# Kernel optimization log

Measured on AMD Instinct MI355X. Metric: run time of the kernel, lower is better.

Reference implementation:

```python
import jax, jax.numpy as jnp
import numpy as np

KH = KW = 3
STRIDE = 1
PAD = 1
DIL = 1


def setup_inputs() -> dict:
    key = jax.random.key(0)
    k0, k1, k2, k3 = jax.random.split(key, 4)
    B, C, H, W = 4, 64, 128, 128
    Cout = 64
    K = KH * KW
    x = jax.random.normal(k0, (B, C, H, W), jnp.float32)
    # main deform-conv weight [Cout, C, KH, KW]
    weight = jax.random.normal(k1, (Cout, C, KH, KW), jnp.float32) * (1.0 / np.sqrt(C * K))
    bias = jax.random.normal(k2, (Cout,), jnp.float32) * 0.01
    # offset-generating conv: 2*K output channels (dy,dx per kernel tap), deform_groups=1
    offset_weight = jax.random.normal(k3, (2 * K, C, KH, KW), jnp.float32) * 0.01
    offset_bias = jnp.zeros((2 * K,), jnp.float32)
    return {"x": x, "weight": weight, "bias": bias,
            "offset_weight": offset_weight, "offset_bias": offset_bias}


def _conv(x, w, b):
    out = jax.lax.conv_general_dilated(
        x, w, (STRIDE, STRIDE), [(PAD, PAD), (PAD, PAD)],
        rhs_dilation=(DIL, DIL), dimension_numbers=("NCHW", "OIHW", "NCHW"))
    return out + b[None, :, None, None]


def _deform_conv(x, weight, bias, offset_weight, offset_bias):
    B, C, H, W = x.shape
    K = KH * KW
    # offsets from sibling conv: [B, 2K, Ho, Wo], layout (k, [dy, dx]) interleaved
    offs = _conv(x, offset_weight, offset_bias)
    Ho, Wo = offs.shape[2], offs.shape[3]
    offs = offs.reshape(B, K, 2, Ho, Wo)
    dy, dx = offs[:, :, 0], offs[:, :, 1]          # [B, K, Ho, Wo]

    # base sampling grid: output pixel origin + dilated kernel tap + learned offset
    base_h = (jnp.arange(Ho) * STRIDE - PAD).astype(x.dtype)
    base_w = (jnp.arange(Wo) * STRIDE - PAD).astype(x.dtype)
    ky, kx = jnp.meshgrid(jnp.arange(KH) * DIL, jnp.arange(KW) * DIL, indexing="ij")
    ky = ky.reshape(K).astype(x.dtype)
    kx = kx.reshape(K).astype(x.dtype)
    py = base_h[None, None, :, None] + ky[None, :, None, None] + dy   # [B,K,Ho,Wo]
    px = base_w[None, None, None, :] + kx[None, :, None, None] + dx

    y0 = jnp.floor(py)
    x0 = jnp.floor(px)
    ly = py - y0   # fractional weights
    lx = px - x0
    y0i = y0.astype(jnp.int32)
    x0i = x0.astype(jnp.int32)

    x_flat = x.reshape(B, C, H * W)

    def gather(yi, xi):
        # zero padding outside the image
        valid = (yi >= 0) & (yi < H) & (xi >= 0) & (xi < W)
        yc = jnp.clip(yi, 0, H - 1)
        xc = jnp.clip(xi, 0, W - 1)
        idx = (yc * W + xc).reshape(B, -1)          # [B, K*Ho*Wo]
        g = jax.vmap(lambda f, i: f[:, i])(x_flat, idx)  # [B, C, K*Ho*Wo]
        g = g.reshape(B, C, K, Ho, Wo)
        return g * valid[:, None].astype(x.dtype)

    v00 = gather(y0i,     x0i)
    v01 = gather(y0i,     x0i + 1)
    v10 = gather(y0i + 1, x0i)
    v11 = gather(y0i + 1, x0i + 1)

    wy = ly[:, None]   # [B,1,K,Ho,Wo]
    wx = lx[:, None]
    patches = (v00 * (1 - wy) * (1 - wx) + v01 * (1 - wy) * wx
               + v10 * wy * (1 - wx) + v11 * wy * wx)   # [B,C,K,Ho,Wo]

    Cout = weight.shape[0]
    out = jnp.einsum("bckhw,ock->bohw", patches, weight.reshape(Cout, C, K))
    return out + bias[None, :, None, None]


def reference(x, weight, bias, offset_weight, offset_bias):
    return _deform_conv(x, weight, bias, offset_weight, offset_bias)
```

## Files before the change

### kernel.cpp

```cpp
#include <hip/hip_runtime.h>

#define B_   4
#define C_   64
#define H_   128
#define W_   128
#define OC_  64
#define K_   9
#define OCH_ 18
#define CK_  576

#define S_    104
#define WCOLS 768
#define XSW   72
#define XSH   7
#define XSC   (XSH*XSW)
#define XSC1  (3*XSW)
#define XSB   4096
#define NS2   1008
#define NS1   432

#define WPAD_HALFS  (OC_*WCOLS)
#define W0PAD_HALFS (32*WCOLS)
#define ZPAGE_BYTE  (2*WPAD_HALFS + 2*W0PAD_HALFS)

using half8v  = __attribute__((ext_vector_type(8))) _Float16;
using half2v  = __attribute__((ext_vector_type(2))) _Float16;
using float4v = __attribute__((ext_vector_type(4))) float;

#define GLDS16(SRC, DST)                                              \
    __builtin_amdgcn_global_load_lds(                                 \
        (__attribute__((address_space(1))) void*)(SRC),               \
        (__attribute__((address_space(3))) void*)(DST), 16, 0, 0)

__global__ void k0_prep(const float* __restrict__ w, const float* __restrict__ ow,
                        _Float16* __restrict__ wpad, _Float16* __restrict__ w0pad,
                        float* __restrict__ zp) {
    if (blockIdx.x == 0 && threadIdx.x < 64) zp[threadIdx.x] = 0.f;
    int i = blockIdx.x * 256 + threadIdx.x;
    if (i < OC_ * WCOLS) {
        int oc = i / WCOLS, col = i - oc * WCOLS;
        int cc = col / 96, r = col - cc * 96;
        int kk = r >> 3, cl = r & 7;
        float v = 0.f;
        if (kk < 9) v = w[oc * CK_ + (cc * 8 + cl) * 9 + kk];
        wpad[i] = (_Float16)v;
    } else {
        int j = i - OC_ * WCOLS;
        if (j < 32 * WCOLS) {
            int rr = j / WCOLS, col = j - rr * WCOLS;
            int cc = col / 96, r = col - cc * 96;
            int kk = r >> 3, cl = r & 7;
            float v = 0.f;
            if (rr < OCH_ && kk < 9) v = ow[rr * CK_ + (cc * 8 + cl) * 9 + kk];
            w0pad[j] = (_Float16)v;
        }
    }
}

__global__ __launch_bounds__(256, 3) void k_fused(
    const float* __restrict__ x, const _Float16* __restrict__ wpad,
    const _Float16* __restrict__ w0pad, const float* __restrict__ bias,
    const float* __restrict__ ob, const float* __restrict__ zp,
    float* __restrict__ out)
{
    __shared__ __align__(16) float    xs[2 * XSB];
    __shared__ __align__(16) _Float16 Pl[64 * S_];
    __shared__ float offs_lds[OCH_ * 64];

    const int g   = blockIdx.x;
    const int xcd = g & 7;
    const int n   = g >> 3;
    const int hb  = n & 1;
    const int hol = (n >> 1) & 15;
    const int b   = n >> 5;
    const int ho  = xcd * 16 + hol;

    const int t = threadIdx.x, lane = t & 63, w = t >> 6;
    const int lr = lane & 15, q = lane >> 4;
    const int lpix = w * 16 + lr;
    const int po   = hb * 64 + lpix;
    const int start = hb * 64 - 4;
    const float* xb = x + ((long)b << 20);

    for (int i = t; i < 64 * 12; i += 256) {
        int row = i / 12, j = i - row * 12;
        *(unsigned*)&Pl[row * S_ + 72 + 2 * j] = 0u;
    }

    int g1o[2]; bool g1k[2], g1v[2];
#pragma unroll
    for (int s = 0; s < 2; s++) {
        int idx = t + 256 * s;
        g1v[s] = idx < NS1;
        int ii = g1v[s] ? idx : 0;
        int c  = ii / 54, rj = ii - c * 54;
        int r3 = rj / 18, jc = rj - r3 * 18;
        int gy = ho - 1 + r3, gx = start + 4 * jc;
        g1k[s] = ((unsigned)gy < (unsigned)H_) && (gx >= 0) && (gx + 3 < W_);
        g1o[s] = (c << 14) + (gy << 7) + gx;
    }
    int g2o[4]; bool g2k[4], g2v[4];
#pragma unroll
    for (int s = 0; s < 4; s++) {
        int idx = t + 256 * s;
        g2v[s] = idx < NS2;
        int ii = g2v[s] ? idx : 0;
        int c  = ii / 126, rj = ii - c * 126;
        int r  = rj / 18, jc = rj - r * 18;
        int gy = ho - 3 + r, gx = start + 4 * jc;
        g2k[s] = ((unsigned)gy < (unsigned)H_) && (gx >= 0) && (gx + 3 < W_);
        g2o[s] = (c << 14) + (gy << 7) + gx;
    }

#pragma unroll
    for (int s = 0; s < 2; s++) if (g1v[s])
        GLDS16(g1k[s] ? (xb + g1o[s]) : zp, xs + 4 * (t + 256 * s));

    float4v oa0 = {0.f,0.f,0.f,0.f}, oa1 = {0.f,0.f,0.f,0.f};

    for (int cc = 0; cc < 8; cc++) {
        __syncthreads();
        if (cc < 7) {
            float* dst = xs + ((cc + 1) & 1) * XSB;
            const float* srcb = xb + ((long)(cc + 1) << 17);
#pragma unroll
            for (int s = 0; s < 2; s++) if (g1v[s])
                GLDS16(g1k[s] ? (srcb + g1o[s]) : zp, dst + 4 * (t + 256 * s));
        }
        {
            const float* b0 = xs + (cc & 1) * XSB + (2 * q) * XSC1;
            const float* b1 = b0 + XSC1;
#pragma unroll
            for (int ky = 0; ky < 3; ky++) {
#pragma unroll
                for (int kx = 0; kx < 3; kx++) {
                    float u0 = b0[ky * XSW + lpix + 3 + kx];
                    float u1 = b1[ky * XSW + lpix + 3 + kx];
                    half2v hv = {(_Float16)u0, (_Float16)u1};
                    *(half2v*)&Pl[lpix * S_ + (ky * 3 + kx) * 8 + 2 * q] = hv;
                }
            }
        }
        __syncthreads();
#pragma unroll
        for (int ks = 0; ks < 3; ks++) {
            half8v a0 = *(const half8v*)&w0pad[lr * WCOLS + cc * 96 + ks * 32 + q * 8];
            half8v a1 = *(const half8v*)&w0pad[(16 + lr) * WCOLS + cc * 96 + ks * 32 + q * 8];
            half8v bv = *(const half8v*)&Pl[lpix * S_ + ks * 32 + q * 8];
            oa0 = __builtin_amdgcn_mfma_f32_16x16x32_f16(a0, bv, oa0, 0, 0, 0);
            oa1 = __builtin_amdgcn_mfma_f32_16x16x32_f16(a1, bv, oa1, 0, 0, 0);
        }
    }

#pragma unroll
    for (int r = 0; r < 4; r++) {
        int ch = q * 4 + r;
        offs_lds[ch * 64 + lpix] = oa0[r] + ob[ch];
    }
#pragma unroll
    for (int r = 0; r < 4; r++) {
        int ch = 16 + q * 4 + r;
        if (ch < OCH_) offs_lds[ch * 64 + lpix] = oa1[r] + ob[ch];
    }
    __syncthreads();

#pragma unroll
    for (int s = 0; s < 4; s++) if (g2v[s])
        GLDS16(g2k[s] ? (xb + g2o[s]) : zp, xs + 4 * (t + 256 * s));

    unsigned moff[9];
    float mw0[9], mw1[9], mw2[9], mw3[9];
    unsigned okm = 0;
#pragma unroll
    for (int kk = 0; kk < 9; kk++) {
        int ky = kk / 3, kx = kk - 3 * ky;
        float dy = offs_lds[(2 * kk) * 64 + lpix];
        float dx = offs_lds[(2 * kk + 1) * 64 + lpix];
        float py = (float)(ho - 1 + ky) + dy;
        float px = (float)(po - 1 + kx) + dx;
        float fy = floorf(py), fx = floorf(px);
        float ly = py - fy, lx = px - fx;
        int y0 = (int)fy, x0 = (int)fx;
        int y1 = y0 + 1, x1 = x0 + 1;
        float vy0 = ((unsigned)y0 < (unsigned)H_) ? 1.f : 0.f;
        float vy1 = ((unsigned)y1 < (unsigned)H_) ? 1.f : 0.f;
        float vx0 = ((unsigned)x0 < (unsigned)W_) ? 1.f : 0.f;
        float vx1 = ((unsigned)x1 < (unsigned)W_) ? 1.f : 0.f;
        float w00 = (1.f - ly) * (1.f - lx) * vy0 * vx0;
        float w01 = (1.f - ly) * lx * vy0 * vx1;
        float w10 = ly * (1.f - lx) * vy1 * vx0;
        float w11 = ly * lx * vy1 * vx1;
        int cy0 = min(max(y0, 0), H_ - 1);
        int cy1 = min(max(y1, 0), H_ - 1);
        int xl  = min(max(x0, 0), W_ - 2);
        bool noswap = (x0 == xl);
        mw0[kk] = noswap ? w00 : w01;
        mw1[kk] = noswap ? w01 : w00;
        mw2[kk] = noswap ? w10 : w11;
        mw3[kk] = noswap ? w11 : w10;
        int sy0 = cy0 - (ho - 3);
        int sy1 = cy1 - (ho - 3);
        int sx  = xl - start;
        bool ok = ((unsigned)sy0 < (unsigned)XSH) && ((unsigned)sy1 < (unsigned)XSH)
               && ((unsigned)sx < (unsigned)(XSW - 1));
        okm |= (ok ? 1u : 0u) << kk;
        moff[kk] = (unsigned)(sy0 * XSW + sx) | ((unsigned)(sy1 * XSW + sx) << 16);
    }

    float4v a00 = {0.f,0.f,0.f,0.f}, a01 = {0.f,0.f,0.f,0.f};
    float4v a10 = {0.f,0.f,0.f,0.f}, a11 = {0.f,0.f,0.f,0.f};
    const int wm = w & 1, wn = w >> 1;

    for (int cc = 0; cc < 8; cc++) {
        __syncthreads();
        if (cc < 7) {
            float* dst = xs + ((cc + 1) & 1) * XSB;
            const float* srcb = xb + ((long)(cc + 1) << 17);
#pragma unroll
            for (int s = 0; s < 4; s++) if (g2v[s])
                GLDS16(g2k[s] ? (srcb + g2o[s]) : zp, dst + 4 * (t + 256 * s));
        }
        const float* xs0 = xs + (cc & 1) * XSB + (2 * q) * XSC;
        const float* xs1 = xs0 + XSC;
        if (__all(okm == 0x1FFu)) {
#pragma unroll
            for (int kk = 0; kk < 9; kk++) {
                int A  = (int)(moff[kk] & 0xFFFFu);
                int Bo = (int)(moff[kk] >> 16);
                float p0 = xs0[A] * mw0[kk] + xs0[A + 1] * mw1[kk]
                         + xs0[Bo] * mw2[kk] + xs0[Bo + 1] * mw3[kk];
                float p1 = xs1[A] * mw0[kk] + xs1[A + 1] * mw1[kk]
                         + xs1[Bo] * mw2[kk] + xs1[Bo + 1] * mw3[kk];
                half2v hv = {(_Float16)p0, (_Float16)p1};
                *(half2v*)&Pl[lpix * S_ + kk * 8 + 2 * q] = hv;
            }
        } else {
            const float* xc0 = xb + ((long)(cc * 8 + 2 * q) << 14);
            const float* xc1 = xc0 + (1 << 14);
#pragma unroll
            for (int kk = 0; kk < 9; kk++) {
                int ky = kk / 3, kx = kk - 3 * ky;
                float dy = offs_lds[(2 * kk) * 64 + lpix];
                float dx = offs_lds[(2 * kk + 1) * 64 + lpix];
                float py = (float)(ho - 1 + ky) + dy;
                float px = (float)(po - 1 + kx) + dx;
                int y0 = (int)floorf(py), x0 = (int)floorf(px);
                int cy0 = min(max(y0, 0), H_ - 1);
                int cy1 = min(max(y0 + 1, 0), H_ - 1);
                int xl  = min(max(x0, 0), W_ - 2);
                int ga = (cy0 << 7) + xl, gb = (cy1 << 7) + xl;
                float p0 = xc0[ga] * mw0[kk] + xc0[ga + 1] * mw1[kk]
                         + xc0[gb] * mw2[kk] + xc0[gb + 1] * mw3[kk];
                float p1 = xc1[ga] * mw0[kk] + xc1[ga + 1] * mw1[kk]
                         + xc1[gb] * mw2[kk] + xc1[gb + 1] * mw3[kk];
                half2v hv = {(_Float16)p0, (_Float16)p1};
                *(half2v*)&Pl[lpix * S_ + kk * 8 + 2 * q] = hv;
            }
        }
        __syncthreads();
#pragma unroll
        for (int ks = 0; ks < 3; ks++) {
            half8v A0 = *(const half8v*)&wpad[(wm * 32 + lr) * WCOLS + cc * 96 + ks * 32 + q * 8];
            half8v A1 = *(const half8v*)&wpad[(wm * 32 + 16 + lr) * WCOLS + cc * 96 + ks * 32 + q * 8];
            half8v B0 = *(const half8v*)&Pl[(wn * 32 + lr) * S_ + ks * 32 + q * 8];
            half8v B1 = *(const half8v*)&Pl[(wn * 32 + 16 + lr) * S_ + ks * 32 + q * 8];
            a00 = __builtin_amdgcn_mfma_f32_16x16x32_f16(A0, B0, a00, 0, 0, 0);
            a01 = __builtin_amdgcn_mfma_f32_16x16x32_f16(A0, B1, a01, 0, 0, 0);
            a10 = __builtin_amdgcn_mfma_f32_16x16x32_f16(A1, B0, a10, 0, 0, 0);
            a11 = __builtin_amdgcn_mfma_f32_16x16x32_f16(A1, B1, a11, 0, 0, 0);
        }
    }

    const int pixc = hb * 64 + wn * 32 + lr;
#pragma unroll
    for (int r = 0; r < 4; r++) {
        int oc0 = wm * 32 + q * 4 + r;
        int oc1 = oc0 + 16;
        float* o0 = out + (((long)(b * OC_ + oc0)) << 14) + (ho << 7);
        float* o1 = out + (((long)(b * OC_ + oc1)) << 14) + (ho << 7);
        o0[pixc]      = a00[r] + bias[oc0];
        o0[pixc + 16] = a01[r] + bias[oc0];
        o1[pixc]      = a10[r] + bias[oc1];
        o1[pixc + 16] = a11[r] + bias[oc1];
    }
}

extern "C" void kernel_launch(void* const* d_in, const int* in_sizes, int n_in,
                              void* d_out, int out_size, void* d_ws, size_t ws_size,
                              hipStream_t stream) {
    const float* x  = (const float*)d_in[0];
    const float* wt = (const float*)d_in[1];
    const float* bi = (const float*)d_in[2];
    const float* ow = (const float*)d_in[3];
    const float* ob = (const float*)d_in[4];
    float* out = (float*)d_out;

    _Float16* wpad  = (_Float16*)d_ws;
    _Float16* w0pad = wpad + WPAD_HALFS;
    float*    zp    = (float*)((char*)d_ws + ZPAGE_BYTE);

    k0_prep<<<(OC_ * WCOLS + 32 * WCOLS + 255) / 256, 256, 0, stream>>>(wt, ow, wpad, w0pad, zp);
    k_fused<<<B_ * H_ * 2, 256, 0, stream>>>(x, wpad, w0pad, bi, ob, zp, out);
}
```

Measured before the change: 152.7 us.

## Shrink deform-stage LDS halo to 5 rows with per-tap global fallback

The staged input window for the deformable sampling stage shrinks from 7 rows to 5 rows per channel, which cuts LDS footprint and the number of async global-to-LDS loads per chunk. The wave-wide all-or-nothing fast path becomes a per-tap fallback: every tap reads LDS at a clamped offset, and only out-of-window taps recompute and read global memory. The barrier moves to the end of each chunk iteration. Offsets above about one pixel now take the slower global path more often, and the divergent per-tap branch adds some cost.

```diff
diff --git a/kernel.cpp b/kernel.cpp
--- a/kernel.cpp
+++ b/kernel.cpp
@@ -12,11 +12,13 @@
 #define S_    104
 #define WCOLS 768
 #define XSW   72
-#define XSH   7
-#define XSC   (XSH*XSW)
+#define XSH2  5
+#define XSC2  (XSH2*XSW)
+#define CHF   (8*XSC2)
 #define XSC1  (3*XSW)
-#define XSB   4096
-#define NS2   1008
+#define XSB1  1728
+#define XSTOT (2*CHF)
+#define NS2   720
 #define NS1   432
 
 #define WPAD_HALFS  (OC_*WCOLS)
@@ -63,7 +65,7 @@
     const float* __restrict__ ob, const float* __restrict__ zp,
     float* __restrict__ out)
 {
-    __shared__ __align__(16) float    xs[2 * XSB];
+    __shared__ __align__(16) float    xs[XSTOT];
     __shared__ __align__(16) _Float16 Pl[64 * S_];
     __shared__ float offs_lds[OCH_ * 64];
 
@@ -99,15 +101,15 @@
         g1k[s] = ((unsigned)gy < (unsigned)H_) && (gx >= 0) && (gx + 3 < W_);
         g1o[s] = (c << 14) + (gy << 7) + gx;
     }
-    int g2o[4]; bool g2k[4], g2v[4];
-#pragma unroll
-    for (int s = 0; s < 4; s++) {
+    int g2o[3]; bool g2k[3], g2v[3];
+#pragma unroll
+    for (int s = 0; s < 3; s++) {
         int idx = t + 256 * s;
         g2v[s] = idx < NS2;
         int ii = g2v[s] ? idx : 0;
-        int c  = ii / 126, rj = ii - c * 126;
+        int c  = ii / 90, rj = ii - c * 90;
         int r  = rj / 18, jc = rj - r * 18;
-        int gy = ho - 3 + r, gx = start + 4 * jc;
+        int gy = ho - 2 + r, gx = start + 4 * jc;
         g2k[s] = ((unsigned)gy < (unsigned)H_) && (gx >= 0) && (gx + 3 < W_);
         g2o[s] = (c << 14) + (gy << 7) + gx;
     }
@@ -121,14 +123,14 @@
     for (int cc = 0; cc < 8; cc++) {
         __syncthreads();
         if (cc < 7) {
-            float* dst = xs + ((cc + 1) & 1) * XSB;
+            float* dst = xs + ((cc + 1) & 1) * XSB1;
             const float* srcb = xb + ((long)(cc + 1) << 17);
 #pragma unroll
             for (int s = 0; s < 2; s++) if (g1v[s])
                 GLDS16(g1k[s] ? (srcb + g1o[s]) : zp, dst + 4 * (t + 256 * s));
         }
         {
-            const float* b0 = xs + (cc & 1) * XSB + (2 * q) * XSC1;
+            const float* b0 = xs + (cc & 1) * XSB1 + (2 * q) * XSC1;
             const float* b1 = b0 + XSC1;
 #pragma unroll
             for (int ky = 0; ky < 3; ky++) {
@@ -165,7 +167,7 @@
     __syncthreads();
 
 #pragma unroll
-    for (int s = 0; s < 4; s++) if (g2v[s])
+    for (int s = 0; s < 3; s++) if (g2v[s])
         GLDS16(g2k[s] ? (xb + g2o[s]) : zp, xs + 4 * (t + 256 * s));
 
     unsigned moff[9];
@@ -198,61 +200,60 @@
         mw1[kk] = noswap ? w01 : w00;
         mw2[kk] = noswap ? w10 : w11;
         mw3[kk] = noswap ? w11 : w10;
-        int sy0 = cy0 - (ho - 3);
-        int sy1 = cy1 - (ho - 3);
+        int sy0 = cy0 - (ho - 2);
+        int sy1 = cy1 - (ho - 2);
         int sx  = xl - start;
-        bool ok = ((unsigned)sy0 < (unsigned)XSH) && ((unsigned)sy1 < (unsigned)XSH)
+        bool ok = ((unsigned)sy0 < (unsigned)XSH2) && ((unsigned)sy1 < (unsigned)XSH2)
                && ((unsigned)sx < (unsigned)(XSW - 1));
         okm |= (ok ? 1u : 0u) << kk;
-        moff[kk] = (unsigned)(sy0 * XSW + sx) | ((unsigned)(sy1 * XSW + sx) << 16);
-    }
+        int syc0 = min(max(sy0, 0), XSH2 - 1);
+        int syc1 = min(max(sy1, 0), XSH2 - 1);
+        int sxc  = min(max(sx, 0), XSW - 2);
+        moff[kk] = (unsigned)(syc0 * XSW + sxc) | ((unsigned)(syc1 * XSW + sxc) << 16);
+    }
+    __syncthreads();
 
     float4v a00 = {0.f,0.f,0.f,0.f}, a01 = {0.f,0.f,0.f,0.f};
     float4v a10 = {0.f,0.f,0.f,0.f}, a11 = {0.f,0.f,0.f,0.f};
     const int wm = w & 1, wn = w >> 1;
 
     for (int cc = 0; cc < 8; cc++) {
-        __syncthreads();
         if (cc < 7) {
-            float* dst = xs + ((cc + 1) & 1) * XSB;
+            float* dst = xs + ((cc + 1) & 1) * CHF;
             const float* srcb = xb + ((long)(cc + 1) << 17);
 #pragma unroll
-            for (int s = 0; s < 4; s++) if (g2v[s])
+            for (int s = 0; s < 3; s++) if (g2v[s])
                 GLDS16(g2k[s] ? (srcb + g2o[s]) : zp, dst + 4 * (t + 256 * s));
         }
-        const float* xs0 = xs + (cc & 1) * XSB + (2 * q) * XSC;
-        const float* xs1 = xs0 + XSC;
-        if (__all(okm == 0x1FFu)) {
+        {
+            const float* x0p = xs + (cc & 1) * CHF + (2 * q) * XSC2;
+            const float* x1p = x0p + XSC2;
+            const float* xc0 = xb + ((long)(cc * 8 + 2 * q) << 14);
+            const float* xc1 = xc0 + (1 << 14);
 #pragma unroll
             for (int kk = 0; kk < 9; kk++) {
                 int A  = (int)(moff[kk] & 0xFFFFu);
                 int Bo = (int)(moff[kk] >> 16);
-                float p0 = xs0[A] * mw0[kk] + xs0[A + 1] * mw1[kk]
-                         + xs0[Bo] * mw2[kk] + xs0[Bo + 1] * mw3[kk];
-                float p1 = xs1[A] * mw0[kk] + xs1[A + 1] * mw1[kk]
-                         + xs1[Bo] * mw2[kk] + xs1[Bo + 1] * mw3[kk];
-                half2v hv = {(_Float16)p0, (_Float16)p1};
-                *(half2v*)&Pl[lpix * S_ + kk * 8 + 2 * q] = hv;
-            }
-        } else {
-            const float* xc0 = xb + ((long)(cc * 8 + 2 * q) << 14);
-            const float* xc1 = xc0 + (1 << 14);
-#pragma unroll
-            for (int kk = 0; kk < 9; kk++) {
-                int ky = kk / 3, kx = kk - 3 * ky;
-                float dy = offs_lds[(2 * kk) * 64 + lpix];
-                float dx = offs_lds[(2 * kk + 1) * 64 + lpix];
-                float py = (float)(ho - 1 + ky) + dy;
-                float px = (float)(po - 1 + kx) + dx;
-                int y0 = (int)floorf(py), x0 = (int)floorf(px);
-                int cy0 = min(max(y0, 0), H_ - 1);
-                int cy1 = min(max(y0 + 1, 0), H_ - 1);
-                int xl  = min(max(x0, 0), W_ - 2);
-                int ga = (cy0 << 7) + xl, gb = (cy1 << 7) + xl;
-                float p0 = xc0[ga] * mw0[kk] + xc0[ga + 1] * mw1[kk]
-                         + xc0[gb] * mw2[kk] + xc0[gb + 1] * mw3[kk];
-                float p1 = xc1[ga] * mw0[kk] + xc1[ga + 1] * mw1[kk]
-                         + xc1[gb] * mw2[kk] + xc1[gb + 1] * mw3[kk];
+                float p0 = x0p[A] * mw0[kk] + x0p[A + 1] * mw1[kk]
+                         + x0p[Bo] * mw2[kk] + x0p[Bo + 1] * mw3[kk];
+                float p1 = x1p[A] * mw0[kk] + x1p[A + 1] * mw1[kk]
+                         + x1p[Bo] * mw2[kk] + x1p[Bo + 1] * mw3[kk];
+                if (__builtin_expect(!((okm >> kk) & 1u), 0)) {
+                    int ky = kk / 3, kx = kk - 3 * ky;
+                    float dy = offs_lds[(2 * kk) * 64 + lpix];
+                    float dx = offs_lds[(2 * kk + 1) * 64 + lpix];
+                    float py = (float)(ho - 1 + ky) + dy;
+                    float px = (float)(po - 1 + kx) + dx;
+                    int y0 = (int)floorf(py), xq0 = (int)floorf(px);
+                    int cy0 = min(max(y0, 0), H_ - 1);
+                    int cy1 = min(max(y0 + 1, 0), H_ - 1);
+                    int xl  = min(max(xq0, 0), W_ - 2);
+                    int ga = (cy0 << 7) + xl, gb = (cy1 << 7) + xl;
+                    p0 = xc0[ga] * mw0[kk] + xc0[ga + 1] * mw1[kk]
+                       + xc0[gb] * mw2[kk] + xc0[gb + 1] * mw3[kk];
+                    p1 = xc1[ga] * mw0[kk] + xc1[ga + 1] * mw1[kk]
+                       + xc1[gb] * mw2[kk] + xc1[gb + 1] * mw3[kk];
+                }
                 half2v hv = {(_Float16)p0, (_Float16)p1};
                 *(half2v*)&Pl[lpix * S_ + kk * 8 + 2 * q] = hv;
             }
@@ -269,6 +270,7 @@
             a10 = __builtin_amdgcn_mfma_f32_16x16x32_f16(A1, B0, a10, 0, 0, 0);
             a11 = __builtin_amdgcn_mfma_f32_16x16x32_f16(A1, B1, a11, 0, 0, 0);
         }
+        if (cc < 7) __syncthreads();
     }
 
     const int pixc = hb * 64 + wn * 32 + lr;
```

After: 156.1 us. 2.2% more time.
